# Optimization experiments

Hardware: AMD Instinct MI355X
Metric: run time of the kernel (lower is better)

Reference implementation:

```python
import jax, jax.numpy as jnp
import numpy as np

B, T, F = 4096, 9, 553
U1 = 256        # MHCIP_units (bi_gru1)
U23 = 256       # bi_gru2 / bi_gru3 units (hard-coded in source)
W1_UNITS = 512  # attention hidden units
FC_DIM = 512


def _glorot(key, shape):
    fan_in, fan_out = shape[0], shape[-1]
    lim = np.sqrt(6.0 / (fan_in + fan_out)).astype(np.float32)
    return jax.random.uniform(key, shape, jnp.float32, -lim, lim)


def setup_inputs() -> dict:
    key = jax.random.key(0)
    ks = iter(jax.random.split(key, 40))
    d = {}
    d["peptide"] = jax.random.normal(next(ks), (B, T, F), jnp.float32)
    d["hidden"] = jnp.zeros((B, U1), jnp.float32)

    def gru_params(name, in_dim, units):
        d[name + "_W"] = _glorot(next(ks), (in_dim, 3 * units))
        d[name + "_U"] = _glorot(next(ks), (units, 3 * units))
        d[name + "_b"] = jnp.zeros((2, 3 * units), jnp.float32)  # [input_bias, recurrent_bias] (reset_after)

    gru_params("g1f", F, U1)
    gru_params("g1b", F, U1)
    gru_params("g2f", 2 * U1, U23)
    gru_params("g2b", 2 * U1, U23)
    gru_params("g3f", 2 * U23, U23)
    gru_params("g3b", 2 * U23, U23)

    d["att_W1"] = _glorot(next(ks), (2 * U23, W1_UNITS))
    d["att_b1"] = jnp.zeros((W1_UNITS,), jnp.float32)
    d["att_V"] = _glorot(next(ks), (W1_UNITS, 1))
    d["att_bV"] = jnp.zeros((1,), jnp.float32)
    d["fc1_W"] = _glorot(next(ks), (2 * U23, FC_DIM))
    d["fc1_b"] = jnp.zeros((FC_DIM,), jnp.float32)
    d["fc2_W"] = _glorot(next(ks), (FC_DIM, 2))
    d["fc2_b"] = jnp.zeros((2,), jnp.float32)
    return d


def _gru(x, h0, W, U, b):
    # Keras GRU v2 math (reset_after=True): separate input/recurrent biases.
    xp = jnp.einsum('bti,ij->btj', x, W) + b[0]  # precompute input projections [B,T,3U]

    def step(h, xt):
        inner = h @ U + b[1]
        xz, xr, xh = jnp.split(xt, 3, axis=-1)
        iz, ir, ih = jnp.split(inner, 3, axis=-1)
        z = jax.nn.sigmoid(xz + iz)
        r = jax.nn.sigmoid(xr + ir)
        hh = jnp.tanh(xh + r * ih)
        hn = z * h + (1.0 - z) * hh
        return hn, hn

    h_last, ys = jax.lax.scan(step, h0, jnp.swapaxes(xp, 0, 1))  # scan over time
    return jnp.swapaxes(ys, 0, 1), h_last


def _bigru(x, h0f, h0b, Wf, Uf, bf, Wb, Ub, bb):
    yf, hf = _gru(x, h0f, Wf, Uf, bf)
    yb, hb = _gru(x[:, ::-1], h0b, Wb, Ub, bb)  # go_backwards
    return jnp.concatenate([yf, yb[:, ::-1]], axis=-1), hf, hb


def reference(peptide, hidden,
              g1f_W, g1f_U, g1f_b, g1b_W, g1b_U, g1b_b,
              g2f_W, g2f_U, g2f_b, g2b_W, g2b_U, g2b_b,
              g3f_W, g3f_U, g3f_b, g3b_W, g3b_U, g3b_b,
              att_W1, att_b1, att_V, att_bV,
              fc1_W, fc1_b, fc2_W, fc2_b):
    # dropout layers are identity in inference mode
    out, _, _ = _bigru(peptide, hidden, hidden, g1f_W, g1f_U, g1f_b, g1b_W, g1b_U, g1b_b)
    z0 = jnp.zeros((peptide.shape[0], U23), peptide.dtype)
    out, _, _ = _bigru(out, z0, z0, g2f_W, g2f_U, g2f_b, g2b_W, g2b_U, g2b_b)
    out, _, _ = _bigru(out, z0, z0, g3f_W, g3f_U, g3f_b, g3b_W, g3b_U, g3b_b)
    # Bahdanau additive attention pooling
    score = jnp.tanh(out @ att_W1 + att_b1) @ att_V + att_bV     # [B,T,1]
    attention_weights = jax.nn.softmax(score, axis=1)
    context = jnp.sum(attention_weights * out, axis=1)            # [B,512]
    h1 = jax.nn.relu(context @ fc1_W + fc1_b)
    logits = h1 @ fc2_W + fc2_b                                   # [B,2]
    return (logits, attention_weights)
```

## Files before the change

### kernel.cpp

```cpp
#include <hip/hip_runtime.h>
#include <math.h>

#define TT 9

typedef __attribute__((ext_vector_type(8))) short bf16x8;
typedef __attribute__((ext_vector_type(4))) float f32x4;

__device__ __forceinline__ unsigned short f2bf(float x) {
    unsigned int u = __float_as_uint(x);
    unsigned int r = (u + 0x7fffu + ((u >> 16) & 1u)) >> 16;
    return (unsigned short)r;
}
__device__ __forceinline__ float bf2f(unsigned short h) {
    return __uint_as_float((unsigned int)h << 16);
}

__global__ __launch_bounds__(256) void cvta_kernel(
    const float* __restrict__ A, unsigned short* __restrict__ Ah,
    unsigned short* __restrict__ Al, int K, int Kp, unsigned total)
{
    for (unsigned idx = blockIdx.x * 256u + threadIdx.x; idx < total;
         idx += gridDim.x * 256u) {
        unsigned row = idx / (unsigned)Kp;
        unsigned k = idx - row * (unsigned)Kp;
        float v = (k < (unsigned)K) ? A[(size_t)row * K + k] : 0.f;
        unsigned short h = f2bf(v);
        unsigned short l = f2bf(v - bf2f(h));
        Ah[idx] = h;
        Al[idx] = l;
    }
}

struct PrepPtrs { const float* w[7]; const float* u[6]; };

__global__ __launch_bounds__(256) void prep_kernel(
    PrepPtrs p, unsigned short* __restrict__ Wh, unsigned short* __restrict__ Wl,
    unsigned short* __restrict__ Upk)
{
    const int job = blockIdx.y;
    if (job < 7) {
        const int N  = (job == 6) ? 512 : 768;
        const int K  = (job < 2) ? 553 : 512;
        const int Kp = (job < 2) ? 576 : 512;
        const unsigned elems = (unsigned)N * Kp;
        unsigned short* wh = Wh + (size_t)job * 442368;
        unsigned short* wl = Wl + (size_t)job * 442368;
        for (unsigned idx = blockIdx.x * 256u + threadIdx.x; idx < elems;
             idx += gridDim.x * 256u) {
            unsigned n = idx / (unsigned)Kp;
            unsigned k = idx - n * (unsigned)Kp;
            float v = (k < (unsigned)K) ? p.w[job][(size_t)k * N + n] : 0.f;
            unsigned short h = f2bf(v);
            wh[idx] = h;
            wl[idx] = f2bf(v - bf2f(h));
        }
    } else {
        const int ju = job - 7;
        unsigned short* up = Upk + (size_t)ju * 393216;
        const float* U = p.u[ju];
        for (unsigned idx = blockIdx.x * 256u + threadIdx.x; idx < 196608u;
             idx += gridDim.x * 256u) {
            unsigned j = idx & 7u;
            unsigned l = (idx >> 3) & 63u;
            unsigned blk = idx >> 9;
            unsigned k   = (blk / 48u) * 32u + ((l >> 4) << 3) + j;
            unsigned col = (blk % 48u) * 16u + (l & 15u);
            float v = U[(size_t)k * 768 + col];
            unsigned short h = f2bf(v);
            up[(size_t)blk * 1024 + l * 8 + j]       = h;
            up[(size_t)blk * 1024 + 512 + l * 8 + j] = f2bf(v - bf2f(h));
        }
    }
}

__global__ __launch_bounds__(256) void projm_kernel(
    const unsigned short* __restrict__ Ah, const unsigned short* __restrict__ Al,
    const unsigned short* __restrict__ Wh, const unsigned short* __restrict__ Wl,
    const float* __restrict__ bs, float* __restrict__ C, int Kp, int N)
{
    __shared__ unsigned short Ah_s[128][40];
    __shared__ unsigned short Al_s[128][40];
    __shared__ unsigned short Wh_s[128][40];
    __shared__ unsigned short Wl_s[128][40];

    const int tid = threadIdx.x;
    const int m0 = blockIdx.y * 128;
    const int n0 = blockIdx.x * 128;

    const int srow = tid >> 1;
    const int skh  = (tid & 1) * 16;

    const unsigned short* pAh = Ah + (size_t)(m0 + srow) * Kp + skh;
    const unsigned short* pAl = Al + (size_t)(m0 + srow) * Kp + skh;
    const unsigned short* pWh = Wh + (size_t)(n0 + srow) * Kp + skh;
    const unsigned short* pWl = Wl + (size_t)(n0 + srow) * Kp + skh;

    const int w    = tid >> 6;
    const int wr   = (w >> 1) * 64;
    const int wc   = (w & 1) * 64;
    const int lane = tid & 63;
    const int lrow = lane & 15;
    const int kg8  = (lane >> 4) * 8;

    f32x4 acc[4][4];
    #pragma unroll
    for (int m = 0; m < 4; ++m)
        #pragma unroll
        for (int n = 0; n < 4; ++n)
            acc[m][n] = (f32x4){0.f, 0.f, 0.f, 0.f};

    uint4 rAh0 = *(const uint4*)(pAh), rAh1 = *(const uint4*)(pAh + 8);
    uint4 rAl0 = *(const uint4*)(pAl), rAl1 = *(const uint4*)(pAl + 8);
    uint4 rWh0 = *(const uint4*)(pWh), rWh1 = *(const uint4*)(pWh + 8);
    uint4 rWl0 = *(const uint4*)(pWl), rWl1 = *(const uint4*)(pWl + 8);
    pAh += 32; pAl += 32; pWh += 32; pWl += 32;

    const int nsteps = Kp >> 5;
    for (int s = 0; s < nsteps; ++s) {
        __syncthreads();
        *(uint4*)&Ah_s[srow][skh]     = rAh0;
        *(uint4*)&Ah_s[srow][skh + 8] = rAh1;
        *(uint4*)&Al_s[srow][skh]     = rAl0;
        *(uint4*)&Al_s[srow][skh + 8] = rAl1;
        *(uint4*)&Wh_s[srow][skh]     = rWh0;
        *(uint4*)&Wh_s[srow][skh + 8] = rWh1;
        *(uint4*)&Wl_s[srow][skh]     = rWl0;
        *(uint4*)&Wl_s[srow][skh + 8] = rWl1;
        __syncthreads();

        if (s + 1 < nsteps) {
            rAh0 = *(const uint4*)(pAh); rAh1 = *(const uint4*)(pAh + 8);
            rAl0 = *(const uint4*)(pAl); rAl1 = *(const uint4*)(pAl + 8);
            rWh0 = *(const uint4*)(pWh); rWh1 = *(const uint4*)(pWh + 8);
            rWl0 = *(const uint4*)(pWl); rWl1 = *(const uint4*)(pWl + 8);
            pAh += 32; pAl += 32; pWh += 32; pWl += 32;
        }

        bf16x8 fa_h[4], fa_l[4], fb_h[4], fb_l[4];
        #pragma unroll
        for (int m = 0; m < 4; ++m) {
            fa_h[m] = *(const bf16x8*)&Ah_s[wr + m * 16 + lrow][kg8];
            fa_l[m] = *(const bf16x8*)&Al_s[wr + m * 16 + lrow][kg8];
        }
        #pragma unroll
        for (int n = 0; n < 4; ++n) {
            fb_h[n] = *(const bf16x8*)&Wh_s[wc + n * 16 + lrow][kg8];
            fb_l[n] = *(const bf16x8*)&Wl_s[wc + n * 16 + lrow][kg8];
        }
        #pragma unroll
        for (int m = 0; m < 4; ++m)
            #pragma unroll
            for (int n = 0; n < 4; ++n) {
                acc[m][n] = __builtin_amdgcn_mfma_f32_16x16x32_bf16(fa_h[m], fb_h[n], acc[m][n], 0, 0, 0);
                acc[m][n] = __builtin_amdgcn_mfma_f32_16x16x32_bf16(fa_h[m], fb_l[n], acc[m][n], 0, 0, 0);
                acc[m][n] = __builtin_amdgcn_mfma_f32_16x16x32_bf16(fa_l[m], fb_h[n], acc[m][n], 0, 0, 0);
            }
    }

    const int orow = (lane >> 4) * 4;
    const int ocol = lane & 15;
    #pragma unroll
    for (int n = 0; n < 4; ++n) {
        const int col = n0 + wc + n * 16 + ocol;
        const float bn = bs[col];
        #pragma unroll
        for (int m = 0; m < 4; ++m) {
            const int rbase = m0 + wr + m * 16 + orow;
            #pragma unroll
            for (int r = 0; r < 4; ++r)
                C[(size_t)(rbase + r) * N + col] = acc[m][n][r] + bn;
        }
    }
}

__global__ __launch_bounds__(256) void gru_mfma_kernel(
    const float* __restrict__ xp, const unsigned short* __restrict__ Upk,
    const float* __restrict__ b, const float* __restrict__ h0,
    unsigned short* __restrict__ yh, unsigned short* __restrict__ yl,
    int out_off, int dir)
{
    __shared__ float h[16][272];
    __shared__ float g8[8][772];

    const int tid  = threadIdx.x;
    const int lane = tid & 63;
    const int w    = tid >> 6;
    const int lrow = lane & 15;
    const int lk8  = (lane >> 4) * 8;
    const int r0   = blockIdx.x * 16;

    #pragma unroll
    for (int i = 0; i < 16; ++i)
        h[i][tid] = h0 ? h0[(size_t)(r0 + i) * 256 + tid] : 0.f;

    const float bz = b[768 + tid], br = b[768 + 256 + tid], bhv = b[768 + 512 + tid];
    __syncthreads();

    for (int t = 0; t < TT; ++t) {
        const int te = dir ? (TT - 1 - t) : t;

        f32x4 acc[12];
        #pragma unroll
        for (int j = 0; j < 12; ++j) acc[j] = (f32x4){0.f, 0.f, 0.f, 0.f};

        for (int kt = 0; kt < 8; ++kt) {
            float4 a0 = *(const float4*)&h[lrow][kt * 32 + lk8];
            float4 a1 = *(const float4*)&h[lrow][kt * 32 + lk8 + 4];
            float av[8] = {a0.x, a0.y, a0.z, a0.w, a1.x, a1.y, a1.z, a1.w};
            bf16x8 ah, al;
            #pragma unroll
            for (int e = 0; e < 8; ++e) {
                unsigned short hi = f2bf(av[e]);
                ah[e] = (short)hi;
                al[e] = (short)f2bf(av[e] - bf2f(hi));
            }
            #pragma unroll
            for (int j = 0; j < 12; ++j) {
                const int ntg = w * 12 + j;
                const unsigned short* fb = Upk + ((size_t)(kt * 48 + ntg)) * 1024 + lane * 8;
                bf16x8 bh = *(const bf16x8*)(fb);
                bf16x8 bl = *(const bf16x8*)(fb + 512);
                acc[j] = __builtin_amdgcn_mfma_f32_16x16x32_bf16(ah, bh, acc[j], 0, 0, 0);
                acc[j] = __builtin_amdgcn_mfma_f32_16x16x32_bf16(ah, bl, acc[j], 0, 0, 0);
                acc[j] = __builtin_amdgcn_mfma_f32_16x16x32_bf16(al, bh, acc[j], 0, 0, 0);
            }
        }

        if (lane < 32) {
            const int rowb = (lane >> 4) * 4;
            #pragma unroll
            for (int j = 0; j < 12; ++j) {
                const int col = w * 192 + j * 16 + lrow;
                #pragma unroll
                for (int r = 0; r < 4; ++r)
                    g8[rowb + r][col] = acc[j][r];
            }
        }
        __syncthreads();
        #pragma unroll
        for (int i = 0; i < 8; ++i) {
            const size_t xb = ((size_t)(r0 + i) * TT + te) * 768;
            float xz = xp[xb + tid];
            float xr = xp[xb + tid + 256];
            float xh = xp[xb + tid + 512];
            float z  = 1.f / (1.f + expf(-(xz + g8[i][tid] + bz)));
            float r_ = 1.f / (1.f + expf(-(xr + g8[i][tid + 256] + br)));
            float hh = tanhf(xh + r_ * (g8[i][tid + 512] + bhv));
            float hn = z * h[i][tid] + (1.f - z) * hh;
            h[i][tid] = hn;
            const size_t yi = ((size_t)(r0 + i) * TT + te) * 512 + out_off + tid;
            unsigned short hb = f2bf(hn);
            yh[yi] = hb;
            yl[yi] = f2bf(hn - bf2f(hb));
        }
        __syncthreads();

        if (lane >= 32) {
            const int rowb = ((lane >> 4) - 2) * 4;
            #pragma unroll
            for (int j = 0; j < 12; ++j) {
                const int col = w * 192 + j * 16 + lrow;
                #pragma unroll
                for (int r = 0; r < 4; ++r)
                    g8[rowb + r][col] = acc[j][r];
            }
        }
        __syncthreads();
        #pragma unroll
        for (int i = 0; i < 8; ++i) {
            const int row = i + 8;
            const size_t xb = ((size_t)(r0 + row) * TT + te) * 768;
            float xz = xp[xb + tid];
            float xr = xp[xb + tid + 256];
            float xh = xp[xb + tid + 512];
            float z  = 1.f / (1.f + expf(-(xz + g8[i][tid] + bz)));
            float r_ = 1.f / (1.f + expf(-(xr + g8[i][tid + 256] + br)));
            float hh = tanhf(xh + r_ * (g8[i][tid + 512] + bhv));
            float hn = z * h[row][tid] + (1.f - z) * hh;
            h[row][tid] = hn;
            const size_t yi = ((size_t)(r0 + row) * TT + te) * 512 + out_off + tid;
            unsigned short hb = f2bf(hn);
            yh[yi] = hb;
            yl[yi] = f2bf(hn - bf2f(hb));
        }
        __syncthreads();
    }
}

__global__ __launch_bounds__(64) void tail_kernel(
    const float* __restrict__ H, const unsigned short* __restrict__ Yh,
    const unsigned short* __restrict__ Yl,
    const float* __restrict__ V, const float* __restrict__ bV,
    float* __restrict__ ctx, float* __restrict__ att)
{
    const int b = blockIdx.x;
    const int lane = threadIdx.x;

    float sc[TT];
    #pragma unroll
    for (int t = 0; t < TT; ++t) {
        const float* Hp = H + ((size_t)b * TT + t) * 512;
        float s = 0.f;
        #pragma unroll
        for (int j = 0; j < 8; ++j) {
            int cix = lane + j * 64;
            s = fmaf(tanhf(Hp[cix]), V[cix], s);
        }
        #pragma unroll
        for (int off = 32; off > 0; off >>= 1) s += __shfl_xor(s, off);
        sc[t] = s + bV[0];
    }
    float m = sc[0];
    #pragma unroll
    for (int t = 1; t < TT; ++t) m = fmaxf(m, sc[t]);
    float sum = 0.f;
    float wt[TT];
    #pragma unroll
    for (int t = 0; t < TT; ++t) { wt[t] = expf(sc[t] - m); sum += wt[t]; }
    const float inv = 1.f / sum;
    #pragma unroll
    for (int t = 0; t < TT; ++t) {
        wt[t] *= inv;
        if (lane == t) att[(size_t)b * TT + t] = wt[t];
    }
    #pragma unroll
    for (int j = 0; j < 8; ++j) {
        int cix = lane + j * 64;
        float a = 0.f;
        #pragma unroll
        for (int t = 0; t < TT; ++t) {
            size_t yi = ((size_t)b * TT + t) * 512 + cix;
            a = fmaf(wt[t], bf2f(Yh[yi]) + bf2f(Yl[yi]), a);
        }
        ctx[(size_t)b * 512 + cix] = a;
    }
}

__global__ __launch_bounds__(256) void fc_kernel(
    const float* __restrict__ ctx, const float* __restrict__ W1, const float* __restrict__ b1,
    const float* __restrict__ W2, const float* __restrict__ b2,
    float* __restrict__ logits)
{
    __shared__ float clds[16][512];
    const int tid = threadIdx.x;
    const int r0 = blockIdx.x * 16;
    for (int idx = tid; idx < 16 * 512; idx += 256)
        clds[idx >> 9][idx & 511] = ctx[(size_t)r0 * 512 + idx];
    __syncthreads();

    float acc0[16], acc1[16];
    #pragma unroll
    for (int i = 0; i < 16; ++i) { acc0[i] = 0.f; acc1[i] = 0.f; }

    for (int k = 0; k < 512; k += 8) {
        float w[8][2];
        #pragma unroll
        for (int kk = 0; kk < 8; ++kk) {
            const float* Wr = W1 + (size_t)(k + kk) * 512;
            w[kk][0] = Wr[tid];
            w[kk][1] = Wr[tid + 256];
        }
        #pragma unroll
        for (int i = 0; i < 16; ++i) {
            float4 y0 = *(const float4*)&clds[i][k];
            float4 y1 = *(const float4*)&clds[i][k + 4];
            float yv[8] = {y0.x, y0.y, y0.z, y0.w, y1.x, y1.y, y1.z, y1.w};
            float s0 = acc0[i], s1 = acc1[i];
            #pragma unroll
            for (int kk = 0; kk < 8; ++kk) {
                s0 = fmaf(yv[kk], w[kk][0], s0);
                s1 = fmaf(yv[kk], w[kk][1], s1);
            }
            acc0[i] = s0; acc1[i] = s1;
        }
    }
    const float w2a0 = W2[(size_t)tid * 2],         w2a1 = W2[(size_t)tid * 2 + 1];
    const float w2b0 = W2[(size_t)(tid + 256) * 2], w2b1 = W2[(size_t)(tid + 256) * 2 + 1];
    const float c0 = b1[tid], c1 = b1[tid + 256];
    __syncthreads();
    #pragma unroll
    for (int i = 0; i < 16; ++i) {
        float h0v = fmaxf(acc0[i] + c0, 0.f);
        float h1v = fmaxf(acc1[i] + c1, 0.f);
        clds[i][tid * 2]     = fmaf(h0v, w2a0, h1v * w2b0);
        clds[i][tid * 2 + 1] = fmaf(h0v, w2a1, h1v * w2b1);
    }
    __syncthreads();
    const int wave = tid >> 6, lane = tid & 63;
    for (int i = wave * 4; i < wave * 4 + 4; ++i) {
        float px = clds[i][lane * 2]     + clds[i][(lane + 64) * 2]     + clds[i][(lane + 128) * 2]     + clds[i][(lane + 192) * 2];
        float py = clds[i][lane * 2 + 1] + clds[i][(lane + 64) * 2 + 1] + clds[i][(lane + 128) * 2 + 1] + clds[i][(lane + 192) * 2 + 1];
        #pragma unroll
        for (int off = 32; off > 0; off >>= 1) { px += __shfl_down(px, off); py += __shfl_down(py, off); }
        if (lane == 0) {
            logits[(size_t)(r0 + i) * 2]     = px + b2[0];
            logits[(size_t)(r0 + i) * 2 + 1] = py + b2[1];
        }
    }
}

extern "C" void kernel_launch(void* const* d_in, const int* in_sizes, int n_in,
                              void* d_out, int out_size, void* d_ws, size_t ws_size,
                              hipStream_t stream)
{
    const float* peptide = (const float*)d_in[0];
    const float* hidden  = (const float*)d_in[1];
    const float* gW[6] = { (const float*)d_in[2],  (const float*)d_in[5],
                           (const float*)d_in[8],  (const float*)d_in[11],
                           (const float*)d_in[14], (const float*)d_in[17] };
    const float* gU[6] = { (const float*)d_in[3],  (const float*)d_in[6],
                           (const float*)d_in[9],  (const float*)d_in[12],
                           (const float*)d_in[15], (const float*)d_in[18] };
    const float* gB[6] = { (const float*)d_in[4],  (const float*)d_in[7],
                           (const float*)d_in[10], (const float*)d_in[13],
                           (const float*)d_in[16], (const float*)d_in[19] };
    const float* att_W1 = (const float*)d_in[20];
    const float* att_b1 = (const float*)d_in[21];
    const float* att_V  = (const float*)d_in[22];
    const float* att_bV = (const float*)d_in[23];
    const float* fc1_W = (const float*)d_in[24];
    const float* fc1_b = (const float*)d_in[25];
    const float* fc2_W = (const float*)d_in[26];
    const float* fc2_b = (const float*)d_in[27];

    float* out = (float*)d_out;

    const size_t WJOB = 442368;
    const size_t UJOB = 393216;
    int NC = 1;
    size_t CB = 4096;
    for (; NC <= 32; NC *= 2) {
        CB = 4096 / NC;
        size_t bytes = (size_t)CB * TT * 768 * 4
                     + 2 * (size_t)CB * TT * 512 * 2
                     + 2 * (size_t)CB * TT * 576 * 2
                     + 2 * 7 * WJOB * 2 + 6 * UJOB * 2;
        if (bytes <= ws_size) break;
    }
    if (NC > 32) { NC = 32; CB = 128; }

    char* ws = (char*)d_ws;
    float* xp  = (float*)ws;                                  ws += (size_t)CB * TT * 768 * 4;
    unsigned short* yAh = (unsigned short*)ws;                ws += (size_t)CB * TT * 512 * 2;
    unsigned short* yAl = (unsigned short*)ws;                ws += (size_t)CB * TT * 512 * 2;
    unsigned short* Aph = (unsigned short*)ws;                ws += (size_t)CB * TT * 576 * 2;
    unsigned short* Apl = (unsigned short*)ws;                ws += (size_t)CB * TT * 576 * 2;
    unsigned short* Wh  = (unsigned short*)ws;                ws += 7 * WJOB * 2;
    unsigned short* Wl  = (unsigned short*)ws;                ws += 7 * WJOB * 2;
    unsigned short* Upk = (unsigned short*)ws;
    unsigned short* yBh = Aph;
    unsigned short* yBl = Apl;
    float* H   = xp;
    float* ctx = (float*)Aph;

    const int M = (int)CB * TT;
    dim3 pb(256), pg768(6, M / 128), pg512(4, M / 128);
    dim3 gb(256), gg((unsigned)CB / 16);
    dim3 cab(256);

    PrepPtrs pp;
    for (int i = 0; i < 6; ++i) { pp.w[i] = gW[i]; pp.u[i] = gU[i]; }
    pp.w[6] = att_W1;
    prep_kernel<<<dim3(1728, 13), cab, 0, stream>>>(pp, Wh, Wl, Upk);

    for (int c = 0; c < NC; ++c) {
        const float* pep_c = peptide + (size_t)c * CB * TT * 553;
        const float* hid_c = hidden + (size_t)c * CB * 256;
        float* logits_c = out + (size_t)c * CB * 2;
        float* att_c    = out + 8192 + (size_t)c * CB * TT;

        cvta_kernel<<<dim3(2048), cab, 0, stream>>>(pep_c, Aph, Apl, 553, 576, (unsigned)M * 576u);
        projm_kernel<<<pg768, pb, 0, stream>>>(Aph, Apl, Wh + 0 * WJOB, Wl + 0 * WJOB, gB[0], xp, 576, 768);
        gru_mfma_kernel<<<gg, gb, 0, stream>>>(xp, Upk + 0 * UJOB, gB[0], hid_c, yAh, yAl, 0, 0);
        projm_kernel<<<pg768, pb, 0, stream>>>(Aph, Apl, Wh + 1 * WJOB, Wl + 1 * WJOB, gB[1], xp, 576, 768);
        gru_mfma_kernel<<<gg, gb, 0, stream>>>(xp, Upk + 1 * UJOB, gB[1], hid_c, yAh, yAl, 256, 1);

        projm_kernel<<<pg768, pb, 0, stream>>>(yAh, yAl, Wh + 2 * WJOB, Wl + 2 * WJOB, gB[2], xp, 512, 768);
        gru_mfma_kernel<<<gg, gb, 0, stream>>>(xp, Upk + 2 * UJOB, gB[2], nullptr, yBh, yBl, 0, 0);
        projm_kernel<<<pg768, pb, 0, stream>>>(yAh, yAl, Wh + 3 * WJOB, Wl + 3 * WJOB, gB[3], xp, 512, 768);
        gru_mfma_kernel<<<gg, gb, 0, stream>>>(xp, Upk + 3 * UJOB, gB[3], nullptr, yBh, yBl, 256, 1);

        projm_kernel<<<pg768, pb, 0, stream>>>(yBh, yBl, Wh + 4 * WJOB, Wl + 4 * WJOB, gB[4], xp, 512, 768);
        gru_mfma_kernel<<<gg, gb, 0, stream>>>(xp, Upk + 4 * UJOB, gB[4], nullptr, yAh, yAl, 0, 0);
        projm_kernel<<<pg768, pb, 0, stream>>>(yBh, yBl, Wh + 5 * WJOB, Wl + 5 * WJOB, gB[5], xp, 512, 768);
        gru_mfma_kernel<<<gg, gb, 0, stream>>>(xp, Upk + 5 * UJOB, gB[5], nullptr, yAh, yAl, 256, 1);

        projm_kernel<<<pg512, pb, 0, stream>>>(yAh, yAl, Wh + 6 * WJOB, Wl + 6 * WJOB, att_b1, H, 512, 512);
        tail_kernel<<<dim3((unsigned)CB), dim3(64), 0, stream>>>(H, yAh, yAl, att_V, att_bV, ctx, att_c);
        fc_kernel<<<dim3((unsigned)CB / 16), dim3(256), 0, stream>>>(ctx, fc1_W, fc1_b, fc2_W, fc2_b, logits_c);
    }
}
```

Measured before the change: 2.434 ms.

## Batch both GRU directions per launch and double-buffer recurrent weights

Forward and backward GRU directions and their input projections now run in one launch each, selected by blockIdx.y/z, with separate xp buffers so both directions' projections are kept. Inside the GRU step, the recurrent weight fragments are software-pipelined with two register buffers, and the xp gate inputs are prefetched into registers before the MFMA loop. Launch bounds request two blocks per CU. The workspace layout changes so the ping-pong y buffers alias the projection input buffers. The aim is to cut launch count, raise occupancy and hide global-load latency. The cost is more register pressure and a larger xp footprint, which may force more batch chunks.

```diff
diff --git a/kernel.cpp b/kernel.cpp
--- a/kernel.cpp
+++ b/kernel.cpp
@@ -75,9 +75,17 @@
 
 __global__ __launch_bounds__(256) void projm_kernel(
     const unsigned short* __restrict__ Ah, const unsigned short* __restrict__ Al,
-    const unsigned short* __restrict__ Wh, const unsigned short* __restrict__ Wl,
-    const float* __restrict__ bs, float* __restrict__ C, int Kp, int N)
-{
+    const unsigned short* __restrict__ Wh0, const unsigned short* __restrict__ Wl0,
+    const float* __restrict__ b0, float* __restrict__ C0,
+    const unsigned short* __restrict__ Wh1, const unsigned short* __restrict__ Wl1,
+    const float* __restrict__ b1, float* __restrict__ C1,
+    int Kp, int N)
+{
+    const unsigned short* Wh = blockIdx.z ? Wh1 : Wh0;
+    const unsigned short* Wl = blockIdx.z ? Wl1 : Wl0;
+    const float* bs = blockIdx.z ? b1 : b0;
+    float* C = blockIdx.z ? C1 : C0;
+
     __shared__ unsigned short Ah_s[128][40];
     __shared__ unsigned short Al_s[128][40];
     __shared__ unsigned short Wh_s[128][40];
@@ -173,14 +181,42 @@
     }
 }
 
-__global__ __launch_bounds__(256) void gru_mfma_kernel(
-    const float* __restrict__ xp, const unsigned short* __restrict__ Upk,
-    const float* __restrict__ b, const float* __restrict__ h0,
-    unsigned short* __restrict__ yh, unsigned short* __restrict__ yl,
-    int out_off, int dir)
+__device__ __forceinline__ void load_group(const unsigned short* __restrict__ base,
+                                           bf16x8* buf)
+{
+    #pragma unroll
+    for (int jj = 0; jj < 6; ++jj) {
+        buf[jj * 2]     = *(const bf16x8*)(base + (size_t)jj * 1024);
+        buf[jj * 2 + 1] = *(const bf16x8*)(base + (size_t)jj * 1024 + 512);
+    }
+}
+
+__device__ __forceinline__ void mfma_group(const bf16x8& ah, const bf16x8& al,
+                                           const bf16x8* buf, f32x4* accg)
+{
+    #pragma unroll
+    for (int jj = 0; jj < 6; ++jj) {
+        accg[jj] = __builtin_amdgcn_mfma_f32_16x16x32_bf16(ah, buf[jj * 2],     accg[jj], 0, 0, 0);
+        accg[jj] = __builtin_amdgcn_mfma_f32_16x16x32_bf16(ah, buf[jj * 2 + 1], accg[jj], 0, 0, 0);
+        accg[jj] = __builtin_amdgcn_mfma_f32_16x16x32_bf16(al, buf[jj * 2],     accg[jj], 0, 0, 0);
+    }
+}
+
+__global__ __launch_bounds__(256, 2) void gru_mfma_kernel(
+    const float* __restrict__ xpf, const float* __restrict__ xpb,
+    const unsigned short* __restrict__ Upk0, const unsigned short* __restrict__ Upk1,
+    const float* __restrict__ bb0, const float* __restrict__ bb1,
+    const float* __restrict__ h0,
+    unsigned short* __restrict__ yh, unsigned short* __restrict__ yl)
 {
     __shared__ float h[16][272];
     __shared__ float g8[8][772];
+
+    const int dir = blockIdx.y;
+    const float* xp = dir ? xpb : xpf;
+    const unsigned short* Upk = dir ? Upk1 : Upk0;
+    const float* b = dir ? bb1 : bb0;
+    const int out_off = dir ? 256 : 0;
 
     const int tid  = threadIdx.x;
     const int lane = tid & 63;
@@ -199,11 +235,26 @@
     for (int t = 0; t < TT; ++t) {
         const int te = dir ? (TT - 1 - t) : t;
 
+        float x1[24];
+        #pragma unroll
+        for (int i = 0; i < 8; ++i) {
+            const float* xr_ = xp + ((size_t)(r0 + i) * TT + te) * 768 + tid;
+            x1[i * 3 + 0] = xr_[0];
+            x1[i * 3 + 1] = xr_[256];
+            x1[i * 3 + 2] = xr_[512];
+        }
+
         f32x4 acc[12];
         #pragma unroll
         for (int j = 0; j < 12; ++j) acc[j] = (f32x4){0.f, 0.f, 0.f, 0.f};
 
+        bf16x8 bufA[12], bufB[12];
+        load_group(Upk + ((size_t)(w * 12)) * 1024 + lane * 8, bufA);
+
         for (int kt = 0; kt < 8; ++kt) {
+            const unsigned short* kbase = Upk + ((size_t)(kt * 48 + w * 12)) * 1024 + lane * 8;
+            load_group(kbase + 6 * 1024, bufB);
+
             float4 a0 = *(const float4*)&h[lrow][kt * 32 + lk8];
             float4 a1 = *(const float4*)&h[lrow][kt * 32 + lk8 + 4];
             float av[8] = {a0.x, a0.y, a0.z, a0.w, a1.x, a1.y, a1.z, a1.w};
@@ -214,16 +265,20 @@
                 ah[e] = (short)hi;
                 al[e] = (short)f2bf(av[e] - bf2f(hi));
             }
-            #pragma unroll
-            for (int j = 0; j < 12; ++j) {
-                const int ntg = w * 12 + j;
-                const unsigned short* fb = Upk + ((size_t)(kt * 48 + ntg)) * 1024 + lane * 8;
-                bf16x8 bh = *(const bf16x8*)(fb);
-                bf16x8 bl = *(const bf16x8*)(fb + 512);
-                acc[j] = __builtin_amdgcn_mfma_f32_16x16x32_bf16(ah, bh, acc[j], 0, 0, 0);
-                acc[j] = __builtin_amdgcn_mfma_f32_16x16x32_bf16(ah, bl, acc[j], 0, 0, 0);
-                acc[j] = __builtin_amdgcn_mfma_f32_16x16x32_bf16(al, bh, acc[j], 0, 0, 0);
-            }
+
+            mfma_group(ah, al, bufA, &acc[0]);
+            if (kt + 1 < 8)
+                load_group(kbase + 48 * 1024, bufA);
+            mfma_group(ah, al, bufB, &acc[6]);
+        }
+
+        float x2[24];
+        #pragma unroll
+        for (int i = 0; i < 8; ++i) {
+            const float* xr_ = xp + ((size_t)(r0 + 8 + i) * TT + te) * 768 + tid;
+            x2[i * 3 + 0] = xr_[0];
+            x2[i * 3 + 1] = xr_[256];
+            x2[i * 3 + 2] = xr_[512];
         }
 
         if (lane < 32) {
@@ -239,13 +294,9 @@
         __syncthreads();
         #pragma unroll
         for (int i = 0; i < 8; ++i) {
-            const size_t xb = ((size_t)(r0 + i) * TT + te) * 768;
-            float xz = xp[xb + tid];
-            float xr = xp[xb + tid + 256];
-            float xh = xp[xb + tid + 512];
-            float z  = 1.f / (1.f + expf(-(xz + g8[i][tid] + bz)));
-            float r_ = 1.f / (1.f + expf(-(xr + g8[i][tid + 256] + br)));
-            float hh = tanhf(xh + r_ * (g8[i][tid + 512] + bhv));
+            float z  = 1.f / (1.f + expf(-(x1[i * 3 + 0] + g8[i][tid] + bz)));
+            float r_ = 1.f / (1.f + expf(-(x1[i * 3 + 1] + g8[i][tid + 256] + br)));
+            float hh = tanhf(x1[i * 3 + 2] + r_ * (g8[i][tid + 512] + bhv));
             float hn = z * h[i][tid] + (1.f - z) * hh;
             h[i][tid] = hn;
             const size_t yi = ((size_t)(r0 + i) * TT + te) * 512 + out_off + tid;
@@ -269,13 +320,9 @@
         #pragma unroll
         for (int i = 0; i < 8; ++i) {
             const int row = i + 8;
-            const size_t xb = ((size_t)(r0 + row) * TT + te) * 768;
-            float xz = xp[xb + tid];
-            float xr = xp[xb + tid + 256];
-            float xh = xp[xb + tid + 512];
-            float z  = 1.f / (1.f + expf(-(xz + g8[i][tid] + bz)));
-            float r_ = 1.f / (1.f + expf(-(xr + g8[i][tid + 256] + br)));
-            float hh = tanhf(xh + r_ * (g8[i][tid + 512] + bhv));
+            float z  = 1.f / (1.f + expf(-(x2[i * 3 + 0] + g8[i][tid] + bz)));
+            float r_ = 1.f / (1.f + expf(-(x2[i * 3 + 1] + g8[i][tid + 256] + br)));
+            float hh = tanhf(x2[i * 3 + 2] + r_ * (g8[i][tid + 512] + bhv));
             float hn = z * h[row][tid] + (1.f - z) * hh;
             h[row][tid] = hn;
             const size_t yi = ((size_t)(r0 + row) * TT + te) * 512 + out_off + tid;
@@ -431,8 +478,7 @@
     size_t CB = 4096;
     for (; NC <= 32; NC *= 2) {
         CB = 4096 / NC;
-        size_t bytes = (size_t)CB * TT * 768 * 4
-                     + 2 * (size_t)CB * TT * 512 * 2
+        size_t bytes = 2 * (size_t)CB * TT * 768 * 4
                      + 2 * (size_t)CB * TT * 576 * 2
                      + 2 * 7 * WJOB * 2 + 6 * UJOB * 2;
         if (bytes <= ws_size) break;
@@ -440,22 +486,22 @@
     if (NC > 32) { NC = 32; CB = 128; }
 
     char* ws = (char*)d_ws;
-    float* xp  = (float*)ws;                                  ws += (size_t)CB * TT * 768 * 4;
-    unsigned short* yAh = (unsigned short*)ws;                ws += (size_t)CB * TT * 512 * 2;
-    unsigned short* yAl = (unsigned short*)ws;                ws += (size_t)CB * TT * 512 * 2;
-    unsigned short* Aph = (unsigned short*)ws;                ws += (size_t)CB * TT * 576 * 2;
-    unsigned short* Apl = (unsigned short*)ws;                ws += (size_t)CB * TT * 576 * 2;
+    float* xpf = (float*)ws;                                  ws += (size_t)CB * TT * 768 * 4;
+    float* xpb = (float*)ws;                                  ws += (size_t)CB * TT * 768 * 4;
+    unsigned short* Aph = (unsigned short*)ws;
+    unsigned short* Apl = Aph + (size_t)CB * TT * 576;
+    unsigned short* yh  = Aph;
+    unsigned short* yl  = yh + (size_t)CB * TT * 512;
+    ws += 2 * (size_t)CB * TT * 576 * 2;
     unsigned short* Wh  = (unsigned short*)ws;                ws += 7 * WJOB * 2;
     unsigned short* Wl  = (unsigned short*)ws;                ws += 7 * WJOB * 2;
     unsigned short* Upk = (unsigned short*)ws;
-    unsigned short* yBh = Aph;
-    unsigned short* yBl = Apl;
-    float* H   = xp;
-    float* ctx = (float*)Aph;
+    float* H   = xpf;
+    float* ctx = xpb;
 
     const int M = (int)CB * TT;
-    dim3 pb(256), pg768(6, M / 128), pg512(4, M / 128);
-    dim3 gb(256), gg((unsigned)CB / 16);
+    dim3 pb(256), pg768(6, M / 128, 2), pg512(4, M / 128, 1);
+    dim3 gb(256), gg((unsigned)CB / 16, 2);
     dim3 cab(256);
 
     PrepPtrs pp;
@@ -470,23 +516,28 @@
         float* att_c    = out + 8192 + (size_t)c * CB * TT;
 
         cvta_kernel<<<dim3(2048), cab, 0, stream>>>(pep_c, Aph, Apl, 553, 576, (unsigned)M * 576u);
-        projm_kernel<<<pg768, pb, 0, stream>>>(Aph, Apl, Wh + 0 * WJOB, Wl + 0 * WJOB, gB[0], xp, 576, 768);
-        gru_mfma_kernel<<<gg, gb, 0, stream>>>(xp, Upk + 0 * UJOB, gB[0], hid_c, yAh, yAl, 0, 0);
-        projm_kernel<<<pg768, pb, 0, stream>>>(Aph, Apl, Wh + 1 * WJOB, Wl + 1 * WJOB, gB[1], xp, 576, 768);
-        gru_mfma_kernel<<<gg, gb, 0, stream>>>(xp, Upk + 1 * UJOB, gB[1], hid_c, yAh, yAl, 256, 1);
-
-        projm_kernel<<<pg768, pb, 0, stream>>>(yAh, yAl, Wh + 2 * WJOB, Wl + 2 * WJOB, gB[2], xp, 512, 768);
-        gru_mfma_kernel<<<gg, gb, 0, stream>>>(xp, Upk + 2 * UJOB, gB[2], nullptr, yBh, yBl, 0, 0);
-        projm_kernel<<<pg768, pb, 0, stream>>>(yAh, yAl, Wh + 3 * WJOB, Wl + 3 * WJOB, gB[3], xp, 512, 768);
-        gru_mfma_kernel<<<gg, gb, 0, stream>>>(xp, Upk + 3 * UJOB, gB[3], nullptr, yBh, yBl, 256, 1);
-
-        projm_kernel<<<pg768, pb, 0, stream>>>(yBh, yBl, Wh + 4 * WJOB, Wl + 4 * WJOB, gB[4], xp, 512, 768);
-        gru_mfma_kernel<<<gg, gb, 0, stream>>>(xp, Upk + 4 * UJOB, gB[4], nullptr, yAh, yAl, 0, 0);
-        projm_kernel<<<pg768, pb, 0, stream>>>(yBh, yBl, Wh + 5 * WJOB, Wl + 5 * WJOB, gB[5], xp, 512, 768);
-        gru_mfma_kernel<<<gg, gb, 0, stream>>>(xp, Upk + 5 * UJOB, gB[5], nullptr, yAh, yAl, 256, 1);
-
-        projm_kernel<<<pg512, pb, 0, stream>>>(yAh, yAl, Wh + 6 * WJOB, Wl + 6 * WJOB, att_b1, H, 512, 512);
-        tail_kernel<<<dim3((unsigned)CB), dim3(64), 0, stream>>>(H, yAh, yAl, att_V, att_bV, ctx, att_c);
+        projm_kernel<<<pg768, pb, 0, stream>>>(Aph, Apl,
+            Wh + 0 * WJOB, Wl + 0 * WJOB, gB[0], xpf,
+            Wh + 1 * WJOB, Wl + 1 * WJOB, gB[1], xpb, 576, 768);
+        gru_mfma_kernel<<<gg, gb, 0, stream>>>(xpf, xpb, Upk + 0 * UJOB, Upk + 1 * UJOB,
+                                               gB[0], gB[1], hid_c, yh, yl);
+
+        projm_kernel<<<pg768, pb, 0, stream>>>(yh, yl,
+            Wh + 2 * WJOB, Wl + 2 * WJOB, gB[2], xpf,
+            Wh + 3 * WJOB, Wl + 3 * WJOB, gB[3], xpb, 512, 768);
+        gru_mfma_kernel<<<gg, gb, 0, stream>>>(xpf, xpb, Upk + 2 * UJOB, Upk + 3 * UJOB,
+                                               gB[2], gB[3], nullptr, yh, yl);
+
+        projm_kernel<<<pg768, pb, 0, stream>>>(yh, yl,
+            Wh + 4 * WJOB, Wl + 4 * WJOB, gB[4], xpf,
+            Wh + 5 * WJOB, Wl + 5 * WJOB, gB[5], xpb, 512, 768);
+        gru_mfma_kernel<<<gg, gb, 0, stream>>>(xpf, xpb, Upk + 4 * UJOB, Upk + 5 * UJOB,
+                                               gB[4], gB[5], nullptr, yh, yl);
+
+        projm_kernel<<<pg512, pb, 0, stream>>>(yh, yl,
+            Wh + 6 * WJOB, Wl + 6 * WJOB, att_b1, H,
+            Wh + 6 * WJOB, Wl + 6 * WJOB, att_b1, H, 512, 512);
+        tail_kernel<<<dim3((unsigned)CB), dim3(64), 0, stream>>>(H, yh, yl, att_V, att_bV, ctx, att_c);
         fc_kernel<<<dim3((unsigned)CB / 16), dim3(256), 0, stream>>>(ctx, fc1_W, fc1_b, fc2_W, fc2_b, logits_c);
     }
 }
```

New measurement: 2.050 ms. 1.19x faster.
